# Kernel tuning notes

Measured on AMD Instinct MI355X. Metric: run time of the kernel, lower is better.

The kernel has to match this reference:

```python
import jax, jax.numpy as jnp
import numpy as np

B, H, W, C = 4, 64, 64, 128  # input feature map; num_heads == filters == C


def setup_inputs() -> dict:
    key = jax.random.key(0)
    ks = jax.random.split(key, 5)
    x = jax.random.normal(ks[0], (B, H, W, C), dtype=jnp.float32)
    scale = 0.02  # keep QK^T logits in a sane range for softmax
    Wf = jax.random.normal(ks[1], (C, C), dtype=jnp.float32) * scale
    Wg = jax.random.normal(ks[2], (C, C), dtype=jnp.float32) * scale
    Wh = jax.random.normal(ks[3], (C, C), dtype=jnp.float32) * scale
    Wv = jax.random.normal(ks[4], (C, C), dtype=jnp.float32) * scale
    zeros = jnp.zeros((C,), dtype=jnp.float32)
    return {
        "x": x,
        "Wf": Wf, "bf": zeros,
        "Wg": Wg, "bg": zeros,
        "Wh": Wh, "bh": zeros,
        "Wv": Wv, "bv": zeros,
        "gamma": jnp.float32(0.01),
    }


def reference(x, Wf, bf, Wg, bg, Wh, bh, Wv, bv, gamma):
    b, h, w, c = x.shape
    n = h * w
    xf = x.reshape(b, n, c)  # 1x1 conv == per-pixel linear
    f = xf @ Wf + bf  # [b, n, heads]
    g = xf @ Wg + bg
    v = xf @ Wh + bh
    # full spatial self-attention, unscaled logits (as in the original)
    s = jnp.einsum("bnc,bmc->bnm", f, g)  # [b, n, n]
    att = jax.nn.softmax(s, axis=-1)
    ctx = jnp.einsum("bnm,bmc->bnc", att, v)  # [b, n, heads]
    ctx = gamma * ctx
    # 1x1 conv v (linear activation) + residual
    o = ctx @ Wv + bv + xf
    return o.reshape(b, h, w, -1)
```

## Files before the change

### kernel.cpp

```cpp
#include <hip/hip_runtime.h>
#include <hip/hip_bf16.h>


typedef __hip_bfloat16 bf16;
typedef float  floatx4 __attribute__((ext_vector_type(4)));
typedef short  shortx8 __attribute__((ext_vector_type(8)));
typedef short  shortx4 __attribute__((ext_vector_type(4)));

#define CDIM 128
#define NROW 16384
#define NPB  4096
#define LDW  136
#define LDK  72
#define NSPLIT 4
#define KT   16
#define QTILE 128

__device__ __forceinline__ short f2bf(float v) {
    union { __hip_bfloat16 h; short s; } u; u.h = __float2bfloat16(v); return u.s;
}
__device__ __forceinline__ float bf2f(short s) {
    union { short s2; __hip_bfloat16 h; } u; u.s2 = s; return __bfloat162float(u.h);
}

__global__ __launch_bounds__(256) void proj3_kernel(
    const float* __restrict__ x,
    const float* __restrict__ Wf, const float* __restrict__ bf_,
    const float* __restrict__ Wg, const float* __restrict__ bg_,
    const float* __restrict__ Wh, const float* __restrict__ bh_,
    bf16* __restrict__ f, bf16* __restrict__ g, bf16* __restrict__ vT)
{
    __shared__ bf16 wt[128 * LDW];

    const int t    = threadIdx.x;
    const int wave = t >> 6, lane = t & 63;
    const int quad = lane >> 4, l16 = lane & 15;
    const int mtx    = blockIdx.x >> 8;
    const int rowblk = (blockIdx.x & 255) * 64;
    const int row    = rowblk + wave * 16 + l16;

    const float* Ws[3] = {Wf, Wg, Wh};
    const float* Bs[3] = {bf_, bg_, bh_};
    const float* W    = Ws[mtx];
    const float* bias = Bs[mtx];

    for (int i = t; i < 128 * 32; i += 256) {
        int k = i >> 5, n0 = (i & 31) * 4;
        floatx4 wv = *(const floatx4*)(W + k * CDIM + n0);
#pragma unroll
        for (int j = 0; j < 4; ++j)
            *(short*)&wt[(n0 + j) * LDW + k] = f2bf(wv[j]);
    }

    shortx8 afr[4];
    {
        const float* xp = x + (size_t)row * CDIM + quad * 8;
#pragma unroll
        for (int kc = 0; kc < 4; ++kc) {
            floatx4 u = *(const floatx4*)(xp + kc * 32);
            floatx4 w = *(const floatx4*)(xp + kc * 32 + 4);
            shortx8 a;
            a[0]=f2bf(u[0]); a[1]=f2bf(u[1]); a[2]=f2bf(u[2]); a[3]=f2bf(u[3]);
            a[4]=f2bf(w[0]); a[5]=f2bf(w[1]); a[6]=f2bf(w[2]); a[7]=f2bf(w[3]);
            afr[kc] = a;
        }
    }
    __syncthreads();

    floatx4 acc[8];
#pragma unroll
    for (int nt = 0; nt < 8; ++nt) acc[nt] = (floatx4){0.f, 0.f, 0.f, 0.f};
#pragma unroll
    for (int nt = 0; nt < 8; ++nt) {
        const bf16* wrow = &wt[(nt * 16 + l16) * LDW + quad * 8];
#pragma unroll
        for (int kc = 0; kc < 4; ++kc) {
            shortx8 b = *(const shortx8*)(wrow + kc * 32);
            acc[nt] = __builtin_amdgcn_mfma_f32_16x16x32_bf16(afr[kc], b, acc[nt], 0, 0, 0);
        }
    }

    if (mtx < 2) {
        bf16* dst = (mtx == 0) ? f : g;
#pragma unroll
        for (int nt = 0; nt < 8; ++nt) {
            int col = nt * 16 + l16;
            float bv_ = bias[col];
#pragma unroll
            for (int r = 0; r < 4; ++r) {
                int orow = rowblk + wave * 16 + quad * 4 + r;
                *(short*)&dst[(size_t)orow * CDIM + col] = f2bf(acc[nt][r] + bv_);
            }
        }
    } else {
        int orow0 = rowblk + wave * 16 + quad * 4;
        int batch = orow0 >> 12, n = orow0 & 4095;
#pragma unroll
        for (int nt = 0; nt < 8; ++nt) {
            int ch = nt * 16 + l16;
            float bv_ = bias[ch];
            shortx4 pk;
#pragma unroll
            for (int r = 0; r < 4; ++r) pk[r] = f2bf(acc[nt][r] + bv_);
            *(shortx4*)&vT[((size_t)batch * CDIM + ch) * NPB + n] = pk;
        }
    }
}

__global__ __launch_bounds__(256, 2) void attn_kernel(
    const bf16* __restrict__ f, const bf16* __restrict__ g,
    const bf16* __restrict__ vT,
    bf16* __restrict__ Opart, float* __restrict__ lbuf)
{
    __shared__ bf16 gs[64 * LDW];
    __shared__ bf16 vs[128 * LDK];
    __shared__ bf16 ps[4 * 32 * LDK];

    const int t    = threadIdx.x;
    const int wave = t >> 6, lane = t & 63;
    const int quad = lane >> 4, l16 = lane & 15;
    const int qg    = blockIdx.x;
    const int split = blockIdx.y;
    const int b  = qg >> 5;
    const int qt = qg & 31;
    const int qbase = b * NPB + qt * QTILE + wave * 32;

    shortx8 qf[2][4];
#pragma unroll
    for (int sub = 0; sub < 2; ++sub) {
        const bf16* qp = f + (size_t)(qbase + sub * 16 + l16) * CDIM + quad * 8;
#pragma unroll
        for (int kc = 0; kc < 4; ++kc) qf[sub][kc] = *(const shortx8*)(qp + kc * 32);
    }

    floatx4 o[2][8];
#pragma unroll
    for (int sub = 0; sub < 2; ++sub)
#pragma unroll
        for (int ct = 0; ct < 8; ++ct) o[sub][ct] = (floatx4){0.f, 0.f, 0.f, 0.f};
    float lacc[2][4];
#pragma unroll
    for (int sub = 0; sub < 2; ++sub)
#pragma unroll
        for (int r = 0; r < 4; ++r) lacc[sub][r] = 0.f;

    const bf16* gptr = g + (size_t)b * NPB * CDIM;
    const bf16* vptr = vT + (size_t)b * CDIM * NPB;

    const int gkey = t >> 4, gch = (t & 15) * 8;
    const int vch  = t >> 3, vk0 = (t & 7) * 8;

    shortx8 gx[4], vx[4];
    {
        const int kt = split * KT;
#pragma unroll
        for (int i = 0; i < 4; ++i) {
            gx[i] = *(const shortx8*)&gptr[(size_t)(kt * 64 + i * 16 + gkey) * CDIM + gch];
            vx[i] = *(const shortx8*)&vptr[(size_t)(i * 32 + vch) * NPB + kt * 64 + vk0];
        }
    }

    for (int it = 0; it < KT; ++it) {
        __syncthreads();
#pragma unroll
        for (int i = 0; i < 4; ++i) {
            *(shortx8*)&gs[(i * 16 + gkey) * LDW + gch] = gx[i];
            *(shortx8*)&vs[(i * 32 + vch) * LDK + vk0] = vx[i];
        }
        if (it + 1 < KT) {
            const int kt = split * KT + it + 1;
#pragma unroll
            for (int i = 0; i < 4; ++i) {
                gx[i] = *(const shortx8*)&gptr[(size_t)(kt * 64 + i * 16 + gkey) * CDIM + gch];
                vx[i] = *(const shortx8*)&vptr[(size_t)(i * 32 + vch) * NPB + kt * 64 + vk0];
            }
        }
        __syncthreads();

        floatx4 s[2][4];
#pragma unroll
        for (int sub = 0; sub < 2; ++sub)
#pragma unroll
            for (int nt = 0; nt < 4; ++nt) s[sub][nt] = (floatx4){0.f, 0.f, 0.f, 0.f};
#pragma unroll
        for (int nt = 0; nt < 4; ++nt) {
            const bf16* grow = &gs[(nt * 16 + l16) * LDW + quad * 8];
#pragma unroll
            for (int kc = 0; kc < 4; ++kc) {
                shortx8 bfr = *(const shortx8*)(grow + kc * 32);
                s[0][nt] = __builtin_amdgcn_mfma_f32_16x16x32_bf16(qf[0][kc], bfr, s[0][nt], 0, 0, 0);
                s[1][nt] = __builtin_amdgcn_mfma_f32_16x16x32_bf16(qf[1][kc], bfr, s[1][nt], 0, 0, 0);
            }
        }

#pragma unroll
        for (int sub = 0; sub < 2; ++sub) {
            bf16* pw = &ps[(wave * 32 + sub * 16 + quad * 4) * LDK];
#pragma unroll
            for (int r = 0; r < 4; ++r) {
#pragma unroll
                for (int nt = 0; nt < 4; ++nt) {
                    float p = __expf(s[sub][nt][r]);
                    *(short*)&pw[r * LDK + nt * 16 + l16] = f2bf(p);
                    lacc[sub][r] += p;
                }
            }
        }

        shortx8 pa[2][2];
#pragma unroll
        for (int sub = 0; sub < 2; ++sub) {
            const bf16* pr = &ps[(wave * 32 + sub * 16 + l16) * LDK + quad * 8];
            pa[sub][0] = *(const shortx8*)pr;
            pa[sub][1] = *(const shortx8*)(pr + 32);
        }

#pragma unroll
        for (int ct = 0; ct < 8; ++ct) {
            const bf16* vrow = &vs[(ct * 16 + l16) * LDK + quad * 8];
#pragma unroll
            for (int kc2 = 0; kc2 < 2; ++kc2) {
                shortx8 bfr = *(const shortx8*)(vrow + kc2 * 32);
                o[0][ct] = __builtin_amdgcn_mfma_f32_16x16x32_bf16(pa[0][kc2], bfr, o[0][ct], 0, 0, 0);
                o[1][ct] = __builtin_amdgcn_mfma_f32_16x16x32_bf16(pa[1][kc2], bfr, o[1][ct], 0, 0, 0);
            }
        }
    }

    const size_t pbase = ((size_t)qg * NSPLIT + split) * QTILE * CDIM;
#pragma unroll
    for (int sub = 0; sub < 2; ++sub)
#pragma unroll
        for (int ct = 0; ct < 8; ++ct) {
            int col = ct * 16 + l16;
#pragma unroll
            for (int r = 0; r < 4; ++r) {
                int rl = wave * 32 + sub * 16 + quad * 4 + r;
                *(short*)&Opart[pbase + (size_t)rl * CDIM + col] = f2bf(o[sub][ct][r]);
            }
        }
    float* lb = lbuf + ((size_t)qg * NSPLIT + split) * QTILE;
#pragma unroll
    for (int sub = 0; sub < 2; ++sub)
#pragma unroll
        for (int r = 0; r < 4; ++r) {
            float v = lacc[sub][r];
            v += __shfl_xor(v, 1);
            v += __shfl_xor(v, 2);
            v += __shfl_xor(v, 4);
            v += __shfl_xor(v, 8);
            if (l16 == 0) lb[wave * 32 + sub * 16 + quad * 4 + r] = v;
        }
}

__global__ __launch_bounds__(256) void combine_kernel(
    const bf16* __restrict__ Opart, const float* __restrict__ lbuf,
    bf16* __restrict__ ctx)
{
    const int tid  = blockIdx.x * 256 + threadIdx.x;
    const int row  = tid >> 5;
    const int col0 = (tid & 31) * 4;
    const int qg   = row >> 7;
    const int rl   = row & 127;

    float L = 0.f;
#pragma unroll
    for (int s = 0; s < NSPLIT; ++s)
        L += lbuf[((size_t)qg * NSPLIT + s) * QTILE + rl];
    float inv = 1.0f / L;

    float acc[4] = {0.f, 0.f, 0.f, 0.f};
#pragma unroll
    for (int s = 0; s < NSPLIT; ++s) {
        shortx4 v = *(const shortx4*)&Opart[(((size_t)qg * NSPLIT + s) * QTILE + rl) * CDIM + col0];
#pragma unroll
        for (int j = 0; j < 4; ++j) acc[j] += bf2f(v[j]);
    }
    shortx4 outp;
#pragma unroll
    for (int j = 0; j < 4; ++j) outp[j] = f2bf(acc[j] * inv);
    *(shortx4*)&ctx[(size_t)row * CDIM + col0] = outp;
}

__global__ __launch_bounds__(256) void out_kernel(
    const bf16* __restrict__ ctx, const float* __restrict__ Wv,
    const float* __restrict__ bv, const float* __restrict__ x,
    const float* __restrict__ gamma, float* __restrict__ out)
{
    __shared__ bf16 wt[64 * LDW];

    const int t    = threadIdx.x;
    const int wave = t >> 6, lane = t & 63;
    const int quad = lane >> 4, l16 = lane & 15;
    const int rowblk = (blockIdx.x >> 1) * 64;
    const int colblk = (blockIdx.x & 1) * 64;
    const int row    = rowblk + wave * 16 + l16;

    const float gm = gamma[0];
    for (int i = t; i < 128 * 16; i += 256) {
        int k = i >> 4, n0 = (i & 15) * 4 + colblk;
        floatx4 wv4 = *(const floatx4*)(Wv + k * CDIM + n0);
#pragma unroll
        for (int j = 0; j < 4; ++j)
            *(short*)&wt[(n0 - colblk + j) * LDW + k] = f2bf(wv4[j] * gm);
    }

    shortx8 afr[4];
    {
        const bf16* cp = ctx + (size_t)row * CDIM + quad * 8;
#pragma unroll
        for (int kc = 0; kc < 4; ++kc) afr[kc] = *(const shortx8*)(cp + kc * 32);
    }
    __syncthreads();

    floatx4 acc[4];
#pragma unroll
    for (int nt = 0; nt < 4; ++nt) acc[nt] = (floatx4){0.f, 0.f, 0.f, 0.f};
#pragma unroll
    for (int nt = 0; nt < 4; ++nt) {
        const bf16* wrow = &wt[(nt * 16 + l16) * LDW + quad * 8];
#pragma unroll
        for (int kc = 0; kc < 4; ++kc) {
            shortx8 b = *(const shortx8*)(wrow + kc * 32);
            acc[nt] = __builtin_amdgcn_mfma_f32_16x16x32_bf16(afr[kc], b, acc[nt], 0, 0, 0);
        }
    }

#pragma unroll
    for (int nt = 0; nt < 4; ++nt) {
        int col = colblk + nt * 16 + l16;
        float bias = bv[col];
#pragma unroll
        for (int r = 0; r < 4; ++r) {
            int orow = rowblk + wave * 16 + quad * 4 + r;
            size_t idx = (size_t)orow * CDIM + col;
            out[idx] = acc[nt][r] + bias + x[idx];
        }
    }
}

extern "C" void kernel_launch(void* const* d_in, const int* in_sizes, int n_in,
                              void* d_out, int out_size, void* d_ws, size_t ws_size,
                              hipStream_t stream)
{
    const float* x   = (const float*)d_in[0];
    const float* Wf  = (const float*)d_in[1];
    const float* bf_ = (const float*)d_in[2];
    const float* Wg  = (const float*)d_in[3];
    const float* bg_ = (const float*)d_in[4];
    const float* Wh  = (const float*)d_in[5];
    const float* bh_ = (const float*)d_in[6];
    const float* Wv  = (const float*)d_in[7];
    const float* bv  = (const float*)d_in[8];
    const float* gm  = (const float*)d_in[9];
    float* out = (float*)d_out;

    bf16* f     = (bf16*)d_ws;
    bf16* g     = f + (size_t)NROW * CDIM;
    bf16* vT    = g + (size_t)NROW * CDIM;
    bf16* ctx   = vT + (size_t)4 * CDIM * NPB;
    bf16* Opart = ctx + (size_t)NROW * CDIM;
    float* lbuf = (float*)(Opart + (size_t)128 * NSPLIT * QTILE * CDIM);

    proj3_kernel<<<768, 256, 0, stream>>>(x, Wf, bf_, Wg, bg_, Wh, bh_, f, g, vT);
    attn_kernel<<<dim3(128, NSPLIT), 256, 0, stream>>>(f, g, vT, Opart, lbuf);
    combine_kernel<<<2048, 256, 0, stream>>>(Opart, lbuf, ctx);
    out_kernel<<<512, 256, 0, stream>>>(ctx, Wv, bv, x, gm, out);
}
```

Measured before the change: 153.5 us.

## Fuse split-combine into output projection and stage V transpose through shared memory

Drops the separate combine kernel: the output projection kernel now sums the split-K partial outputs, normalises them by the summed softmax denominators and feeds the result straight into its MFMA, so the bf16 ctx tensor is never written to or read back from global memory. Each block now covers all 128 output columns for 64 rows, halving the grid and requiring the full Wv tile in shared memory. The V-projection path now transposes through shared memory and writes vT as 16-byte row segments instead of scattered 8-byte stores. The trade-off is fewer blocks and more LDS per block in the output kernel, plus extra barriers in the projection kernel.

```diff
diff --git a/kernel.cpp b/kernel.cpp
--- a/kernel.cpp
+++ b/kernel.cpp
@@ -93,8 +93,9 @@
             }
         }
     } else {
-        int orow0 = rowblk + wave * 16 + quad * 4;
-        int batch = orow0 >> 12, n = orow0 & 4095;
+        __syncthreads();
+        bf16* vt = wt;
+        const int nloc0 = wave * 16 + quad * 4;
 #pragma unroll
         for (int nt = 0; nt < 8; ++nt) {
             int ch = nt * 16 + l16;
@@ -102,8 +103,18 @@
             shortx4 pk;
 #pragma unroll
             for (int r = 0; r < 4; ++r) pk[r] = f2bf(acc[nt][r] + bv_);
-            *(shortx4*)&vT[((size_t)batch * CDIM + ch) * NPB + n] = pk;
-        }
+            *(shortx4*)&vt[ch * LDK + nloc0] = pk;
+        }
+        __syncthreads();
+        const int ch  = t >> 1;
+        const int seg = (t & 1) * 32;
+        const int batch = rowblk >> 12;
+        const int n0 = (rowblk & 4095) + seg;
+        bf16* dst = &vT[((size_t)batch * CDIM + ch) * NPB + n0];
+        const bf16* src = &vt[ch * LDK + seg];
+#pragma unroll
+        for (int j = 0; j < 4; ++j)
+            *(shortx8*)(dst + j * 8) = *(const shortx8*)(src + j * 8);
     }
 }
 
@@ -253,71 +264,59 @@
         }
 }
 
-__global__ __launch_bounds__(256) void combine_kernel(
+__global__ __launch_bounds__(256) void out_kernel(
     const bf16* __restrict__ Opart, const float* __restrict__ lbuf,
-    bf16* __restrict__ ctx)
+    const float* __restrict__ Wv, const float* __restrict__ bv,
+    const float* __restrict__ x, const float* __restrict__ gamma,
+    float* __restrict__ out)
 {
-    const int tid  = blockIdx.x * 256 + threadIdx.x;
-    const int row  = tid >> 5;
-    const int col0 = (tid & 31) * 4;
-    const int qg   = row >> 7;
-    const int rl   = row & 127;
-
-    float L = 0.f;
-#pragma unroll
-    for (int s = 0; s < NSPLIT; ++s)
-        L += lbuf[((size_t)qg * NSPLIT + s) * QTILE + rl];
-    float inv = 1.0f / L;
-
-    float acc[4] = {0.f, 0.f, 0.f, 0.f};
-#pragma unroll
-    for (int s = 0; s < NSPLIT; ++s) {
-        shortx4 v = *(const shortx4*)&Opart[(((size_t)qg * NSPLIT + s) * QTILE + rl) * CDIM + col0];
-#pragma unroll
-        for (int j = 0; j < 4; ++j) acc[j] += bf2f(v[j]);
-    }
-    shortx4 outp;
-#pragma unroll
-    for (int j = 0; j < 4; ++j) outp[j] = f2bf(acc[j] * inv);
-    *(shortx4*)&ctx[(size_t)row * CDIM + col0] = outp;
-}
-
-__global__ __launch_bounds__(256) void out_kernel(
-    const bf16* __restrict__ ctx, const float* __restrict__ Wv,
-    const float* __restrict__ bv, const float* __restrict__ x,
-    const float* __restrict__ gamma, float* __restrict__ out)
-{
-    __shared__ bf16 wt[64 * LDW];
+    __shared__ bf16 wt[128 * LDW];
 
     const int t    = threadIdx.x;
     const int wave = t >> 6, lane = t & 63;
     const int quad = lane >> 4, l16 = lane & 15;
-    const int rowblk = (blockIdx.x >> 1) * 64;
-    const int colblk = (blockIdx.x & 1) * 64;
+    const int rowblk = blockIdx.x * 64;
     const int row    = rowblk + wave * 16 + l16;
 
     const float gm = gamma[0];
-    for (int i = t; i < 128 * 16; i += 256) {
-        int k = i >> 4, n0 = (i & 15) * 4 + colblk;
+    for (int i = t; i < 128 * 32; i += 256) {
+        int k = i >> 5, n0 = (i & 31) * 4;
         floatx4 wv4 = *(const floatx4*)(Wv + k * CDIM + n0);
 #pragma unroll
         for (int j = 0; j < 4; ++j)
-            *(short*)&wt[(n0 - colblk + j) * LDW + k] = f2bf(wv4[j] * gm);
-    }
+            *(short*)&wt[(n0 + j) * LDW + k] = f2bf(wv4[j] * gm);
+    }
+
+    const int qg = row >> 7, rl = row & 127;
+    float L = 0.f;
+#pragma unroll
+    for (int s = 0; s < NSPLIT; ++s)
+        L += lbuf[((size_t)qg * NSPLIT + s) * QTILE + rl];
+    const float inv = 1.0f / L;
 
     shortx8 afr[4];
-    {
-        const bf16* cp = ctx + (size_t)row * CDIM + quad * 8;
-#pragma unroll
-        for (int kc = 0; kc < 4; ++kc) afr[kc] = *(const shortx8*)(cp + kc * 32);
+#pragma unroll
+    for (int kc = 0; kc < 4; ++kc) {
+        float a8[8] = {0,0,0,0,0,0,0,0};
+#pragma unroll
+        for (int s = 0; s < NSPLIT; ++s) {
+            const bf16* p = &Opart[(((size_t)qg * NSPLIT + s) * QTILE + rl) * CDIM + quad * 8 + kc * 32];
+            shortx8 v = *(const shortx8*)p;
+#pragma unroll
+            for (int j = 0; j < 8; ++j) a8[j] += bf2f(v[j]);
+        }
+        shortx8 a;
+#pragma unroll
+        for (int j = 0; j < 8; ++j) a[j] = f2bf(a8[j] * inv);
+        afr[kc] = a;
     }
     __syncthreads();
 
-    floatx4 acc[4];
-#pragma unroll
-    for (int nt = 0; nt < 4; ++nt) acc[nt] = (floatx4){0.f, 0.f, 0.f, 0.f};
-#pragma unroll
-    for (int nt = 0; nt < 4; ++nt) {
+    floatx4 acc[8];
+#pragma unroll
+    for (int nt = 0; nt < 8; ++nt) acc[nt] = (floatx4){0.f, 0.f, 0.f, 0.f};
+#pragma unroll
+    for (int nt = 0; nt < 8; ++nt) {
         const bf16* wrow = &wt[(nt * 16 + l16) * LDW + quad * 8];
 #pragma unroll
         for (int kc = 0; kc < 4; ++kc) {
@@ -327,8 +326,8 @@
     }
 
 #pragma unroll
-    for (int nt = 0; nt < 4; ++nt) {
-        int col = colblk + nt * 16 + l16;
+    for (int nt = 0; nt < 8; ++nt) {
+        int col = nt * 16 + l16;
         float bias = bv[col];
 #pragma unroll
         for (int r = 0; r < 4; ++r) {
@@ -358,12 +357,10 @@
     bf16* f     = (bf16*)d_ws;
     bf16* g     = f + (size_t)NROW * CDIM;
     bf16* vT    = g + (size_t)NROW * CDIM;
-    bf16* ctx   = vT + (size_t)4 * CDIM * NPB;
-    bf16* Opart = ctx + (size_t)NROW * CDIM;
+    bf16* Opart = vT + (size_t)4 * CDIM * NPB;
     float* lbuf = (float*)(Opart + (size_t)128 * NSPLIT * QTILE * CDIM);
 
     proj3_kernel<<<768, 256, 0, stream>>>(x, Wf, bf_, Wg, bg_, Wh, bh_, f, g, vT);
     attn_kernel<<<dim3(128, NSPLIT), 256, 0, stream>>>(f, g, vT, Opart, lbuf);
-    combine_kernel<<<2048, 256, 0, stream>>>(Opart, lbuf, ctx);
-    out_kernel<<<512, 256, 0, stream>>>(ctx, Wv, bv, x, gm, out);
-}
+    out_kernel<<<256, 256, 0, stream>>>(Opart, lbuf, Wv, bv, x, gm, out);
+}
```

After: 151.7 us. Within noise of the previous version (-1.2%).
